# Optimization experiments

Measured on AMD Instinct MI355X. Metric: run time of the kernel, lower is better.

The kernel has to match this reference:

```python
import jax, jax.numpy as jnp
import numpy as np
from jax import lax

K_STEEP = 10.0      # ssm_K: surrogate spike steepness
V_TH_MIN = 0.1      # ssm_v_th_min
EK_FLOOR = 0.01     # ssm_ek_floor


def setup_inputs() -> dict:
    key = jax.random.key(0)
    ks = jax.random.split(key, 11)
    B, T, D, N = 2, 1024, 1024, 16
    s = lambda fan: 1.0 / np.sqrt(fan)
    return {
        "hidden_states": jax.random.normal(ks[0], (B, T, D), jnp.float32),
        "W_xz": jax.random.normal(ks[1], (D, 2 * D), jnp.float32) * s(D),
        "W_dt": jax.random.normal(ks[2], (D, D), jnp.float32) * s(D),
        "b_dt": jax.random.normal(ks[3], (D,), jnp.float32) * 0.1,
        "A_log": jax.random.uniform(ks[4], (D, N), jnp.float32, 0.0, 1.0),
        "W_B": jax.random.normal(ks[5], (D, N), jnp.float32) * s(D),
        "W_C": jax.random.normal(ks[6], (D, N), jnp.float32) * s(D),
        "D_skip": jax.random.normal(ks[7], (D,), jnp.float32) * 0.1,
        "W_out": jax.random.normal(ks[8], (D, D), jnp.float32) * s(D),
        "v_th": jax.random.uniform(ks[9], (D,), jnp.float32, 0.0, 0.5),
    }


def _bio_ssm(h, W_xz, W_dt, b_dt, A_log, W_B, W_C, D_skip, W_out, v_th):
    # h: (T, B, D) time-major, as in the torch wrapper after permute(1,0,2)
    T, B, D = h.shape
    N = A_log.shape[1]
    xz = jnp.einsum('tbd,de->tbe', h, W_xz)
    x, z = jnp.split(xz, 2, axis=-1)                       # (T,B,D) each
    dt = jax.nn.softplus(jnp.einsum('tbd,de->tbe', x, W_dt) + b_dt)  # (T,B,D)
    A = -jnp.exp(A_log)                                     # (D,N), negative
    Bm = jnp.einsum('tbd,dn->tbn', h, W_B)                  # (T,B,N)
    Cm = jnp.einsum('tbd,dn->tbn', h, W_C)                  # (T,B,N)
    decay = jnp.exp(dt[..., None] * A)                      # (T,B,D,N)
    inp = (dt * x)[..., None] * Bm[:, :, None, :]           # (T,B,D,N)

    def step(s, td):
        dec, ip, c = td
        s = dec * s + ip                                    # (B,D,N)
        y = jnp.einsum('bdn,bn->bd', s, c)
        return s, y

    s0 = jnp.zeros((B, D, N), h.dtype)
    _, y = lax.scan(step, s0, (decay, inp, Cm))             # y: (T,B,D)
    y = y + D_skip * x
    vth = jnp.maximum(v_th, V_TH_MIN)
    spike_p = jax.nn.sigmoid(K_STEEP * (y - vth))           # surrogate spiking gate
    y_sp = y * spike_p
    pc = jnp.mean(spike_p)                                  # ponder cost
    efc = jnp.mean(jax.nn.relu(EK_FLOOR - y * y))           # ek-floor cost
    out = jnp.einsum('tbd,de->tbe', y_sp * jax.nn.silu(z), W_out)
    return out, pc, efc


def reference(hidden_states, W_xz, W_dt, b_dt, A_log, W_B, W_C, D_skip, W_out, v_th):
    h = jnp.transpose(hidden_states, (1, 0, 2))             # (T,B,D)
    h_out, pc, efc = _bio_ssm(h, W_xz, W_dt, b_dt, A_log, W_B, W_C, D_skip, W_out, v_th)
    out = h_out - h                                         # mixer residual delta
    return jnp.transpose(out, (1, 0, 2))                    # (B,T,D)
```

## Files before the change

### kernel.cpp

```cpp
#include <hip/hip_runtime.h>
#include <hip/hip_bf16.h>
#include <stdint.h>

#define TT 1024
#define BB 2
#define DD 1024
#define NN 16
#define NCH 128
#define LCH 8

#define K_STEEP 10.0f
#define V_TH_MIN 0.1f
#define L2E 1.44269504088896f

typedef __bf16 bf16x8 __attribute__((ext_vector_type(8)));
typedef float f32x4 __attribute__((ext_vector_type(4)));

__device__ __forceinline__ short f2bf(float f) {
    union { float f; unsigned u; } c; c.f = f;
    unsigned r = (c.u + 0x7fffu + ((c.u >> 16) & 1u)) >> 16;
    return (short)r;
}
__device__ __forceinline__ float bf2f(short s) {
    union { unsigned u; float f; } c;
    c.u = ((unsigned)(unsigned short)s) << 16;
    return c.f;
}

__device__ __forceinline__ void gload_lds16(const void* g, void* l) {
    __builtin_amdgcn_global_load_lds(
        (const __attribute__((address_space(1))) void*)g,
        (__attribute__((address_space(3))) void*)l, 16, 0, 0);
}

template<int BM, int EPI, bool FUSE_BC>
__global__ __launch_bounds__(256) void gemm_mfma(
    const short* __restrict__ A, int lda,
    const short* __restrict__ BT, int ldb,
    float* __restrict__ C, int ldc,
    int M, int Ncols, int K,
    const float* __restrict__ bias,
    const float* __restrict__ sub,
    short* __restrict__ xb_out,
    short* __restrict__ xzT_out,
    const short* __restrict__ WbcT,
    short* __restrict__ bcs)
{
    constexpr int RI = BM / 32;
    constexpr int AS_SZ = (FUSE_BC && BM * 32 < 2048) ? 2048 : BM * 32;
    __shared__ short As[AS_SZ];
    __shared__ short Bs[128 * 32];

    const int tid = threadIdx.x;
    const int wave = tid >> 6, lane = tid & 63;
    const int kk = (lane >> 4) * 8;
    const int r16 = lane & 15;
    const int wr = wave >> 1, wc = wave & 1;

    if (FUSE_BC && blockIdx.x == gridDim.x - 1) {
        const int bm2 = blockIdx.y * 32;
        f32x4 acc2 = {};
        for (int k0 = 0; k0 < K; k0 += 64) {
            int off = tid * 16;
            int row = off >> 7;
            int ke  = (off & 127) >> 1;
            gload_lds16(A + (size_t)(bm2 + row) * lda + k0 + ke, (char*)As + off);
            gload_lds16(WbcT + (size_t)row * K + k0 + ke, (char*)Bs + off);
            __syncthreads();
            bf16x8 alo = *(const bf16x8*)&As[(wr * 16 + r16) * 64 + kk];
            bf16x8 ahi = *(const bf16x8*)&As[(wr * 16 + r16) * 64 + kk + 32];
            bf16x8 blo = *(const bf16x8*)&Bs[(wc * 16 + r16) * 64 + kk];
            bf16x8 bhi = *(const bf16x8*)&Bs[(wc * 16 + r16) * 64 + kk + 32];
            acc2 = __builtin_amdgcn_mfma_f32_16x16x32_bf16(alo, blo, acc2, 0, 0, 0);
            acc2 = __builtin_amdgcn_mfma_f32_16x16x32_bf16(ahi, bhi, acc2, 0, 0, 0);
            __syncthreads();
        }
        #pragma unroll
        for (int g = 0; g < 4; g++) {
            int row = bm2 + wr * 16 + (lane >> 4) * 4 + g;
            int col = wc * 16 + r16;
            int bb = row >> 10, t = row & 1023;
            int j = t & 7, c = t >> 3;
            bcs[(size_t)(((bb << 3) | j) * NCH + c) * 32 + col] = f2bf(acc2[g]);
        }
        return;
    }

    const int bm = blockIdx.y * BM, bn = blockIdx.x * 128;
    f32x4 acc[RI][4] = {};

    for (int k0 = 0; k0 < K; k0 += 32) {
        #pragma unroll
        for (int it = 0; it < 2; it++) {
            int off = it * 4096 + tid * 16;
            int row = off >> 6;
            int ke  = (off & 63) >> 1;
            gload_lds16(BT + (size_t)(bn + row) * ldb + k0 + ke, (char*)Bs + off);
        }
        if (tid < BM * 4) {
            int off = tid * 16;
            int row = off >> 6;
            int ke  = (off & 63) >> 1;
            gload_lds16(A + (size_t)(bm + row) * lda + k0 + ke, (char*)As + off);
        }
        __syncthreads();

        bf16x8 a[RI], b[4];
        #pragma unroll
        for (int i = 0; i < RI; i++)
            a[i] = *(const bf16x8*)&As[(wr * (BM / 2) + i * 16 + r16) * 32 + kk];
        #pragma unroll
        for (int j = 0; j < 4; j++)
            b[j] = *(const bf16x8*)&Bs[(wc * 64 + j * 16 + r16) * 32 + kk];
        #pragma unroll
        for (int i = 0; i < RI; i++)
            #pragma unroll
            for (int j = 0; j < 4; j++)
                acc[i][j] = __builtin_amdgcn_mfma_f32_16x16x32_bf16(
                    a[i], b[j], acc[i][j], 0, 0, 0);
        __syncthreads();
    }

    #pragma unroll
    for (int i = 0; i < RI; i++) {
        #pragma unroll
        for (int j = 0; j < 4; j++) {
            int row0 = bm + wr * (BM / 2) + i * 16 + (lane >> 4) * 4;
            int col = bn + wc * 64 + j * 16 + r16;
            if (EPI == 3) {
                short4 p;
                #pragma unroll
                for (int g = 0; g < 4; g++) {
                    short h = f2bf(acc[i][j][g]);
                    ((short*)&p)[g] = h;
                    if (col < DD) xb_out[(size_t)(row0 + g) * DD + col] = h;
                }
                *(short4*)&xzT_out[(size_t)col * 2048 + row0] = p;
            } else {
                #pragma unroll
                for (int g = 0; g < 4; g++) {
                    int row = row0 + g;
                    float v = acc[i][j][g];
                    if (EPI == 4) {
                        v += bias[row];
                        v = fmaxf(v, 0.f) + log1pf(__expf(-fabsf(v)));
                    }
                    if (EPI == 2) {
                        v -= sub[(size_t)row * ldc + col];
                    }
                    C[(size_t)row * ldc + col] = v;
                }
            }
        }
    }
}

__device__ __forceinline__ void tr_tile(
    const float* __restrict__ W, short* __restrict__ WT,
    int K, int N, int k0, int n0, int tid)
{
    __shared__ float t[32][33];
    int r = tid >> 3, q = tid & 7;
    float4 v = *(const float4*)&W[(size_t)(k0 + r) * N + n0 + q * 4];
    t[r][q * 4 + 0] = v.x; t[r][q * 4 + 1] = v.y;
    t[r][q * 4 + 2] = v.z; t[r][q * 4 + 3] = v.w;
    __syncthreads();
    short4 o = { f2bf(t[q * 4 + 0][r]), f2bf(t[q * 4 + 1][r]),
                 f2bf(t[q * 4 + 2][r]), f2bf(t[q * 4 + 3][r]) };
    *(short4*)&WT[(size_t)(n0 + r) * K + k0 + q * 4] = o;
}

__global__ __launch_bounds__(256) void prep_all(
    const float* __restrict__ H,    short* __restrict__ Hb,
    const float* __restrict__ W_xz, short* __restrict__ WxzT,
    const float* __restrict__ W_dt, short* __restrict__ WdtT,
    const float* __restrict__ W_out,short* __restrict__ WoutT,
    const float* __restrict__ W_B,  const float* __restrict__ W_C,
    short* __restrict__ WbcT)
{
    int bid = blockIdx.x, tid = threadIdx.x;
    if (bid < 2048) {
        int i = bid * 1024 + tid * 4;
        float4 v = *(const float4*)&H[i];
        short4 o = { f2bf(v.x), f2bf(v.y), f2bf(v.z), f2bf(v.w) };
        *(short4*)&Hb[i] = o;
    } else if (bid < 4096) {
        int t = bid - 2048;
        tr_tile(W_xz, WxzT, DD, 2 * DD, (t >> 6) * 32, (t & 63) * 32, tid);
    } else if (bid < 5120) {
        int t = bid - 4096;
        tr_tile(W_dt, WdtT, DD, DD, (t >> 5) * 32, (t & 31) * 32, tid);
    } else if (bid < 6144) {
        int t = bid - 5120;
        tr_tile(W_out, WoutT, DD, DD, (t >> 5) * 32, (t & 31) * 32, tid);
    } else {
        int g = (bid - 6144) * 256 + tid;
        int k = g & (DD - 1);
        int n = g >> 10;
        float v = (n < 16) ? W_B[(size_t)k * NN + n]
                           : W_C[(size_t)k * NN + n - 16];
        WbcT[(size_t)n * DD + k] = f2bf(v);
    }
}

__global__ __launch_bounds__(256) void tr_g(
    const short* __restrict__ gT, short* __restrict__ gb)
{
    __shared__ short L[64][72];
    const int bt0 = blockIdx.x * 64, d0 = blockIdx.y * 64;
    const int tid = threadIdx.x;
    const int r = tid >> 3, c8 = (tid & 7) * 8;
    #pragma unroll
    for (int p = 0; p < 2; p++) {
        int dd = r + p * 32;
        *(int4*)&L[dd][c8] = *(const int4*)&gT[(size_t)(d0 + dd) * 2048 + bt0 + c8];
    }
    __syncthreads();
    #pragma unroll
    for (int p = 0; p < 2; p++) {
        int tb = r + p * 32;
        short tmp[8];
        #pragma unroll
        for (int k = 0; k < 8; k++) tmp[k] = L[c8 + k][tb];
        *(int4*)&gb[(size_t)(bt0 + tb) * DD + d0 + c8] = *(int4*)&tmp[0];
    }
}

__global__ __launch_bounds__(512) void scan_fused4(
    const float* __restrict__ dtT,
    const short* __restrict__ xzT,
    const short* __restrict__ bcs,
    const float* __restrict__ A_log,
    const float* __restrict__ D_skip,
    const float* __restrict__ v_th,
    short* __restrict__ gT)
{
    __shared__ float Ls[512 * 17];
    __shared__ float Sd[512];
    __shared__ float Gp[8][4][16];
    __shared__ float Gl[8][4][16];
    __shared__ float Gi[8][4][16];

    const int tid = threadIdx.x;
    const int dl = tid & 3;
    const int c  = tid >> 2;
    const int d  = blockIdx.x * 4 + dl;
    const int b  = blockIdx.y;
    const int R0 = b * TT + c * LCH;

    float a2[NN];
    #pragma unroll
    for (int n = 0; n < NN; n++)
        a2[n] = -__expf(A_log[(size_t)d * NN + n]) * L2E;

    float dtv[LCH];
    *(float4*)&dtv[0] = *(const float4*)&dtT[(size_t)d * 2048 + R0];
    *(float4*)&dtv[4] = *(const float4*)&dtT[(size_t)d * 2048 + R0 + 4];
    short xv[LCH], zv[LCH];
    *(int4*)&xv[0] = *(const int4*)&xzT[(size_t)d * 2048 + R0];
    *(int4*)&zv[0] = *(const int4*)&xzT[(size_t)(DD + d) * 2048 + R0];

    float s[NN];
    #pragma unroll
    for (int n = 0; n < NN; n++) s[n] = 0.f;
    float sum_dt = 0.f;

    #pragma unroll
    for (int j = 0; j < LCH; j++) {
        float dt = dtv[j];
        float x  = bf2f(xv[j]);
        float dtx = dt * x;
        sum_dt += dt;
        const short* bp = &bcs[(size_t)(((b << 3) | j) * NCH + c) * 32];
        short bB[NN];
        *(int4*)&bB[0] = *(const int4*)&bp[0];
        *(int4*)&bB[8] = *(const int4*)&bp[8];
        #pragma unroll
        for (int n = 0; n < NN; n++) {
            float dec = exp2f(a2[n] * dt);
            s[n] = fmaf(dec, s[n], dtx * bf2f(bB[n]));
        }
    }
    #pragma unroll
    for (int n = 0; n < NN; n++) Ls[tid * 17 + n] = s[n];
    Sd[tid] = sum_dt;
    __syncthreads();

    {
        int dl2 = tid & 3, n2 = (tid >> 2) & 15, sg = tid >> 6;
        float a2n = -__expf(A_log[(size_t)(blockIdx.x * 4 + dl2) * NN + n2]) * L2E;
        float Pg = 1.f, Lg = 0.f;
        for (int k = 0; k < 16; k++) {
            int lt = (sg * 16 + k) * 4 + dl2;
            float P = exp2f(a2n * Sd[lt]);
            float L = Ls[lt * 17 + n2];
            Lg = fmaf(P, Lg, L);
            Pg *= P;
        }
        Gp[sg][dl2][n2] = Pg; Gl[sg][dl2][n2] = Lg;
        __syncthreads();
        if (tid < 64) {
            int dl3 = tid & 3, n3 = tid >> 2;
            float Sg = 0.f;
            for (int g = 0; g < 8; g++) {
                Gi[g][dl3][n3] = Sg;
                Sg = fmaf(Gp[g][dl3][n3], Sg, Gl[g][dl3][n3]);
            }
        }
        __syncthreads();
        float ss = Gi[sg][dl2][n2];
        for (int k = 0; k < 16; k++) {
            int lt = (sg * 16 + k) * 4 + dl2;
            float P = exp2f(a2n * Sd[lt]);
            float L = Ls[lt * 17 + n2];
            Ls[lt * 17 + n2] = ss;
            ss = fmaf(P, ss, L);
        }
    }
    __syncthreads();

    #pragma unroll
    for (int n = 0; n < NN; n++) s[n] = Ls[tid * 17 + n];

    float dsk = D_skip[d];
    float vth = fmaxf(v_th[d], V_TH_MIN);
    short gvv[LCH];

    #pragma unroll
    for (int j = 0; j < LCH; j++) {
        float dt = dtv[j];
        float x  = bf2f(xv[j]);
        float z  = bf2f(zv[j]);
        float dtx = dt * x;
        const short* bp = &bcs[(size_t)(((b << 3) | j) * NCH + c) * 32];
        short bB[NN], bC[NN];
        *(int4*)&bB[0] = *(const int4*)&bp[0];
        *(int4*)&bB[8] = *(const int4*)&bp[8];
        *(int4*)&bC[0] = *(const int4*)&bp[16];
        *(int4*)&bC[8] = *(const int4*)&bp[24];
        float y = 0.f;
        #pragma unroll
        for (int n = 0; n < NN; n++) {
            float dec = exp2f(a2[n] * dt);
            s[n] = fmaf(dec, s[n], dtx * bf2f(bB[n]));
            y = fmaf(s[n], bf2f(bC[n]), y);
        }
        y = fmaf(dsk, x, y);
        float sp = 1.f / (1.f + __expf(-K_STEEP * (y - vth)));
        float sz = z / (1.f + __expf(-z));
        gvv[j] = f2bf(y * sp * sz);
    }

    *(int4*)&gT[(size_t)d * 2048 + R0] = *(const int4*)&gvv[0];
}

extern "C" void kernel_launch(void* const* d_in, const int* in_sizes, int n_in,
                              void* d_out, int out_size, void* d_ws, size_t ws_size,
                              hipStream_t stream) {
    const float* H      = (const float*)d_in[0];
    const float* W_xz   = (const float*)d_in[1];
    const float* W_dt   = (const float*)d_in[2];
    const float* b_dt   = (const float*)d_in[3];
    const float* A_log  = (const float*)d_in[4];
    const float* W_B    = (const float*)d_in[5];
    const float* W_C    = (const float*)d_in[6];
    const float* D_skip = (const float*)d_in[7];
    const float* W_out  = (const float*)d_in[8];
    const float* v_th   = (const float*)d_in[9];
    float* out = (float*)d_out;

    float* ws  = (float*)d_ws;
    float* dtT = ws;
    short* p16   = (short*)(dtT + 2097152);
    short* bcs   = p16;
    short* xzT   = bcs   + 65536;
    short* xb    = xzT   + 4194304;
    short* Hb    = xb    + 2097152;
    short* WxzT  = Hb    + 2097152;
    short* WdtT  = WxzT  + 2097152;
    short* WoutT = WdtT  + 1048576;
    short* WbcT  = WoutT + 1048576;
    short* gT    = WbcT  + 32768;
    short* gb    = gT    + 2097152;

    const int M = BB * TT;

    prep_all<<<6272, 256, 0, stream>>>(
        H, Hb, W_xz, WxzT, W_dt, WdtT, W_out, WoutT, W_B, W_C, WbcT);
    gemm_mfma<32, 3, true><<<dim3(17, M / 32), 256, 0, stream>>>(
        Hb, DD, WxzT, DD, nullptr, 0, M, 2 * DD, DD,
        nullptr, nullptr, xb, xzT, WbcT, bcs);
    gemm_mfma<32, 4, false><<<dim3(M / 128, DD / 32), 256, 0, stream>>>(
        WdtT, DD, xb, DD, dtT, M, DD, M, DD,
        b_dt, nullptr, nullptr, nullptr, nullptr, nullptr);
    scan_fused4<<<dim3(DD / 4, BB), 512, 0, stream>>>(
        dtT, xzT, bcs, A_log, D_skip, v_th, gT);
    tr_g<<<dim3(2048 / 64, DD / 64), 256, 0, stream>>>(gT, gb);
    gemm_mfma<32, 2, false><<<dim3(DD / 128, M / 32), 256, 0, stream>>>(
        gb, DD, WoutT, DD, out, DD, M, DD, DD,
        nullptr, H, nullptr, nullptr, nullptr, nullptr);
}
```

Before: 116.3 us.

## Compute local chunk outputs in first scan pass, correct with carried-in state

The first pass of the chunked scan now also computes each chunk's local output y assuming zero initial state, and records the cumulative dt. The second pass no longer re-runs the recurrence. It adds the carry-in contribution as sum_n C_n * exp(A_n*cumdt) * s_in[n]. Exponentials go through the hardware exp2 builtin, the sigmoid and SiLU are rewritten in base 2, and the group-prefix buffer reuses Gp in place of a separate Gi array. This trades the second pass's B loads and FMA recurrence for a per-step exp2 and holds yloc/cdt in registers, which may raise register pressure.

```diff
diff --git a/kernel.cpp b/kernel.cpp
--- a/kernel.cpp
+++ b/kernel.cpp
@@ -12,6 +12,15 @@
 #define K_STEEP 10.0f
 #define V_TH_MIN 0.1f
 #define L2E 1.44269504088896f
+
+#if defined(__has_builtin)
+#if __has_builtin(__builtin_amdgcn_exp2f)
+#define EXP2(x) __builtin_amdgcn_exp2f(x)
+#endif
+#endif
+#ifndef EXP2
+#define EXP2(x) exp2f(x)
+#endif
 
 typedef __bf16 bf16x8 __attribute__((ext_vector_type(8)));
 typedef float f32x4 __attribute__((ext_vector_type(4)));
@@ -226,7 +235,7 @@
     }
 }
 
-__global__ __launch_bounds__(512) void scan_fused4(
+__global__ __launch_bounds__(512) void scan_fused5(
     const float* __restrict__ dtT,
     const short* __restrict__ xzT,
     const short* __restrict__ bcs,
@@ -239,7 +248,6 @@
     __shared__ float Sd[512];
     __shared__ float Gp[8][4][16];
     __shared__ float Gl[8][4][16];
-    __shared__ float Gi[8][4][16];
 
     const int tid = threadIdx.x;
     const int dl = tid & 3;
@@ -263,75 +271,15 @@
     float s[NN];
     #pragma unroll
     for (int n = 0; n < NN; n++) s[n] = 0.f;
+    float cdt[LCH], yloc[LCH];
     float sum_dt = 0.f;
 
     #pragma unroll
     for (int j = 0; j < LCH; j++) {
         float dt = dtv[j];
-        float x  = bf2f(xv[j]);
-        float dtx = dt * x;
+        float dtx = dt * bf2f(xv[j]);
         sum_dt += dt;
-        const short* bp = &bcs[(size_t)(((b << 3) | j) * NCH + c) * 32];
-        short bB[NN];
-        *(int4*)&bB[0] = *(const int4*)&bp[0];
-        *(int4*)&bB[8] = *(const int4*)&bp[8];
-        #pragma unroll
-        for (int n = 0; n < NN; n++) {
-            float dec = exp2f(a2[n] * dt);
-            s[n] = fmaf(dec, s[n], dtx * bf2f(bB[n]));
-        }
-    }
-    #pragma unroll
-    for (int n = 0; n < NN; n++) Ls[tid * 17 + n] = s[n];
-    Sd[tid] = sum_dt;
-    __syncthreads();
-
-    {
-        int dl2 = tid & 3, n2 = (tid >> 2) & 15, sg = tid >> 6;
-        float a2n = -__expf(A_log[(size_t)(blockIdx.x * 4 + dl2) * NN + n2]) * L2E;
-        float Pg = 1.f, Lg = 0.f;
-        for (int k = 0; k < 16; k++) {
-            int lt = (sg * 16 + k) * 4 + dl2;
-            float P = exp2f(a2n * Sd[lt]);
-            float L = Ls[lt * 17 + n2];
-            Lg = fmaf(P, Lg, L);
-            Pg *= P;
-        }
-        Gp[sg][dl2][n2] = Pg; Gl[sg][dl2][n2] = Lg;
-        __syncthreads();
-        if (tid < 64) {
-            int dl3 = tid & 3, n3 = tid >> 2;
-            float Sg = 0.f;
-            for (int g = 0; g < 8; g++) {
-                Gi[g][dl3][n3] = Sg;
-                Sg = fmaf(Gp[g][dl3][n3], Sg, Gl[g][dl3][n3]);
-            }
-        }
-        __syncthreads();
-        float ss = Gi[sg][dl2][n2];
-        for (int k = 0; k < 16; k++) {
-            int lt = (sg * 16 + k) * 4 + dl2;
-            float P = exp2f(a2n * Sd[lt]);
-            float L = Ls[lt * 17 + n2];
-            Ls[lt * 17 + n2] = ss;
-            ss = fmaf(P, ss, L);
-        }
-    }
-    __syncthreads();
-
-    #pragma unroll
-    for (int n = 0; n < NN; n++) s[n] = Ls[tid * 17 + n];
-
-    float dsk = D_skip[d];
-    float vth = fmaxf(v_th[d], V_TH_MIN);
-    short gvv[LCH];
-
-    #pragma unroll
-    for (int j = 0; j < LCH; j++) {
-        float dt = dtv[j];
-        float x  = bf2f(xv[j]);
-        float z  = bf2f(zv[j]);
-        float dtx = dt * x;
+        cdt[j] = sum_dt;
         const short* bp = &bcs[(size_t)(((b << 3) | j) * NCH + c) * 32];
         short bB[NN], bC[NN];
         *(int4*)&bB[0] = *(const int4*)&bp[0];
@@ -341,13 +289,76 @@
         float y = 0.f;
         #pragma unroll
         for (int n = 0; n < NN; n++) {
-            float dec = exp2f(a2[n] * dt);
+            float dec = EXP2(a2[n] * dt);
             s[n] = fmaf(dec, s[n], dtx * bf2f(bB[n]));
             y = fmaf(s[n], bf2f(bC[n]), y);
         }
+        yloc[j] = y;
+    }
+    #pragma unroll
+    for (int n = 0; n < NN; n++) Ls[tid * 17 + n] = s[n];
+    Sd[tid] = sum_dt;
+    __syncthreads();
+
+    {
+        int dl2 = tid & 3, n2 = (tid >> 2) & 15, sg = tid >> 6;
+        float a2n = -__expf(A_log[(size_t)(blockIdx.x * 4 + dl2) * NN + n2]) * L2E;
+        float Pg = 1.f, Lg = 0.f;
+        for (int k = 0; k < 16; k++) {
+            int lt = (sg * 16 + k) * 4 + dl2;
+            float P = EXP2(a2n * Sd[lt]);
+            float L = Ls[lt * 17 + n2];
+            Lg = fmaf(P, Lg, L);
+            Pg *= P;
+        }
+        Gp[sg][dl2][n2] = Pg; Gl[sg][dl2][n2] = Lg;
+        __syncthreads();
+        if (tid < 64) {
+            int dl3 = tid & 3, n3 = tid >> 2;
+            float Sg = 0.f;
+            for (int g = 0; g < 8; g++) {
+                float Pgv = Gp[g][dl3][n3];
+                Gp[g][dl3][n3] = Sg;
+                Sg = fmaf(Pgv, Sg, Gl[g][dl3][n3]);
+            }
+        }
+        __syncthreads();
+        float ss = Gp[sg][dl2][n2];
+        for (int k = 0; k < 16; k++) {
+            int lt = (sg * 16 + k) * 4 + dl2;
+            float P = EXP2(a2n * Sd[lt]);
+            float L = Ls[lt * 17 + n2];
+            Ls[lt * 17 + n2] = ss;
+            ss = fmaf(P, ss, L);
+        }
+    }
+    __syncthreads();
+
+    #pragma unroll
+    for (int n = 0; n < NN; n++) s[n] = Ls[tid * 17 + n];
+
+    const float dsk = D_skip[d];
+    const float vth = fmaxf(v_th[d], V_TH_MIN);
+    const float KL2 = K_STEEP * L2E;
+    short gvv[LCH];
+
+    #pragma unroll
+    for (int j = 0; j < LCH; j++) {
+        const short* bp = &bcs[(size_t)(((b << 3) | j) * NCH + c) * 32];
+        short bC[NN];
+        *(int4*)&bC[0] = *(const int4*)&bp[16];
+        *(int4*)&bC[8] = *(const int4*)&bp[24];
+        float y = yloc[j];
+        #pragma unroll
+        for (int n = 0; n < NN; n++) {
+            float e = EXP2(a2[n] * cdt[j]);
+            y = fmaf(bf2f(bC[n]) * e, s[n], y);
+        }
+        float x = bf2f(xv[j]);
+        float z = bf2f(zv[j]);
         y = fmaf(dsk, x, y);
-        float sp = 1.f / (1.f + __expf(-K_STEEP * (y - vth)));
-        float sz = z / (1.f + __expf(-z));
+        float sp = 1.f / (1.f + EXP2(-KL2 * (y - vth)));
+        float sz = z / (1.f + EXP2(-z * L2E));
         gvv[j] = f2bf(y * sp * sz);
     }
 
@@ -393,7 +404,7 @@
     gemm_mfma<32, 4, false><<<dim3(M / 128, DD / 32), 256, 0, stream>>>(
         WdtT, DD, xb, DD, dtT, M, DD, M, DD,
         b_dt, nullptr, nullptr, nullptr, nullptr, nullptr);
-    scan_fused4<<<dim3(DD / 4, BB), 512, 0, stream>>>(
+    scan_fused5<<<dim3(DD / 4, BB), 512, 0, stream>>>(
         dtT, xzT, bcs, A_log, D_skip, v_th, gT);
     tr_g<<<dim3(2048 / 64, DD / 64), 256, 0, stream>>>(gT, gb);
     gemm_mfma<32, 2, false><<<dim3(DD / 128, M / 32), 256, 0, stream>>>(
```

Result: slower. 125.9 us (+8.2%).
